# Performance work log

Hardware: AMD Instinct MI355X
Metric: run time of the kernel (lower is better)

## Reference

```python
import jax, jax.numpy as jnp
import numpy as np

B, N, HID = 1, 2048, 1024
H, WK, WV = 16, 64, 64
DH = HID // H  # 64


def setup_inputs() -> dict:
    key = jax.random.key(0)
    ks = jax.random.split(key, 10)
    s = 0.02
    return {
        "hidden_states": jax.random.normal(ks[0], (B, N, HID), jnp.float32),
        "attention_mask": jnp.ones((B, N), jnp.float32),
        "Wq": jax.random.normal(ks[1], (HID, HID), jnp.float32) * s,
        "bq": jnp.zeros((HID,), jnp.float32),
        "Wk": jax.random.normal(ks[2], (HID, HID), jnp.float32) * s,
        "bk": jnp.zeros((HID,), jnp.float32),
        "Wv": jax.random.normal(ks[3], (HID, HID), jnp.float32) * s,
        "bv": jnp.zeros((HID,), jnp.float32),
        # Conv1D(2*WK+1, DH, bias=False): weight [nx=DH, nf=2*WK+1]
        "W_rel_k": jax.random.normal(ks[4], (DH, 2 * WK + 1), jnp.float32) * s,
        # relative_pos_val: [2*WV+1, DH]
        "W_rel_v": jax.random.normal(ks[5], (2 * WV + 1, DH), jnp.float32) * s,
    }


def _attention(hidden_states, attention_mask, Wq, bq, Wk, bk, Wv, bv, W_rel_k, W_rel_v):
    b, n, _ = hidden_states.shape

    def heads(x):  # [B,N,HID] -> [B,H,N,DH]
        return x.reshape(b, n, H, DH).transpose(0, 2, 1, 3)

    q = heads(hidden_states @ Wq + bq)
    k = heads(hidden_states @ Wk + bk)
    v = heads(hidden_states @ Wv + bv)

    scores = jnp.einsum("bhid,bhjd->bhij", q, k)  # [B,H,N,N]

    # --- relative-position key bias: bias[i, j] = q_i . w_{j-i+WK} for |j-i|<=WK ---
    a_k = jnp.einsum("bhid,dw->bhiw", q, W_rel_k)  # [B,H,N,2*WK+1]
    rows = jnp.arange(n)
    slot = rows[None, :] - rows[:, None] + WK       # [N,N] relative slot j-i+WK
    valid_k = (slot >= 0) & (slot <= 2 * WK)
    bias = a_k[:, :, rows[:, None], jnp.clip(slot, 0, 2 * WK)]  # [B,H,N,N]
    scores = scores + jnp.where(valid_k, bias, 0.0)

    scores = scores / np.float32(np.sqrt(DH))  # temperature == 1.0

    # extended attention mask: (1 - mask) * dtype_min added to scores
    ext = (1.0 - attention_mask)[:, None, None, :] * jnp.finfo(scores.dtype).min
    scores = scores + ext

    probs = jax.nn.softmax(scores, axis=-1)  # [B,H,N,N]

    ctx = jnp.einsum("bhij,bhjd->bhid", probs, v)  # [B,H,N,DH]

    # --- relative-position value: band[i, r] = probs[i, i-WV+r]; ctx += band @ W_rel_v ---
    offs = jnp.arange(2 * WV + 1)
    kpos = rows[:, None] - WV + offs[None, :]       # [N, 2*WV+1] absolute key position
    valid_v = (kpos >= 0) & (kpos < n)
    band = probs[:, :, rows[:, None], jnp.clip(kpos, 0, n - 1)]  # [B,H,N,2*WV+1]
    band = jnp.where(valid_v, band, 0.0)
    ctx = ctx + jnp.einsum("bhiw,wd->bhid", band, W_rel_v)

    # merge heads -> [B,N,HID]
    return ctx.transpose(0, 2, 1, 3).reshape(b, n, HID)


def reference(hidden_states, attention_mask, Wq, bq, Wk, bk, Wv, bv, W_rel_k, W_rel_v):
    return _attention(hidden_states, attention_mask, Wq, bq, Wk, bk, Wv, bv, W_rel_k, W_rel_v)
```

## Files before the change

kernel.cpp:

```cpp
#include <hip/hip_runtime.h>
#include <hip/hip_bf16.h>

#define NSEQ 2048
#define HIDDIM 1024
#define NH 16
#define DHEAD 64
#define NW 129
#define AKS 132
#define VTS 132

typedef float          f32x4 __attribute__((ext_vector_type(4)));
typedef _Float16       f16x4 __attribute__((ext_vector_type(4)));
typedef _Float16       f16x8 __attribute__((ext_vector_type(8)));
typedef unsigned short u16x8 __attribute__((ext_vector_type(8)));
typedef unsigned short u16;

__device__ __forceinline__ float b2f(u16 u){ return __uint_as_float(((unsigned)u) << 16); }
__device__ __forceinline__ float ld_any(const void* p, long idx, int flag){
  return flag ? b2f(((const u16*)p)[idx]) : ((const float*)p)[idx];
}

static const size_t OFF_Q    = 0;
static const size_t OFF_K    = (size_t)4  << 20;
static const size_t OFF_VT   = (size_t)8  << 20;
static const size_t OFF_WT   = (size_t)12 << 20;
static const size_t OFF_AK   = (size_t)18 << 20;
static const size_t OFF_M    = OFF_AK + (size_t)NH * NSEQ * AKS * 4;
static const size_t OFF_L    = OFF_M + (size_t)2 * NH * NSEQ * 4;
static const size_t OFF_CTXP = OFF_L + (size_t)2 * NH * NSEQ * 4;
static const size_t OFF_HSF  = OFF_CTXP + (size_t)2 * NSEQ * HIDDIM * 4;
static const size_t OFF_BIAS = OFF_HSF + (size_t)NSEQ * HIDDIM * 2;
static const size_t OFF_WRK  = OFF_BIAS + 3 * 1024 * 4;
static const size_t OFF_WRV  = OFF_WRK + (size_t)DHEAD * NW * 4;
static const size_t OFF_EXT  = OFF_WRV + (size_t)NW * DHEAD * 4;

__global__ void prep_kernel(const void* __restrict__ hs,
                            const void* __restrict__ Wq, const void* __restrict__ Wk,
                            const void* __restrict__ Wv,
                            const void* __restrict__ bq, const void* __restrict__ bk,
                            const void* __restrict__ bv, const void* __restrict__ wrk,
                            const void* __restrict__ wrv, const void* __restrict__ mask,
                            _Float16* __restrict__ hsf, _Float16* __restrict__ Wt,
                            float* __restrict__ biasf, float* __restrict__ wrkf,
                            float* __restrict__ wrvf, float* __restrict__ extf){
  __shared__ __attribute__((aligned(16))) _Float16 tile[64][65];
  const int flag = (((const unsigned*)mask)[0] == 0x3F800000u) ? 0 : 1;
  const int b = blockIdx.x, t = threadIdx.x;
  if (b < 1024){
    const long base = (long)(b * 256 + t) * 8;
    f16x8 o;
    if (flag){
      const u16* src = (const u16*)hs;
#pragma unroll
      for (int e = 0; e < 8; e++) o[e] = (_Float16)b2f(src[base + e]);
    } else {
      const float* src = (const float*)hs;
#pragma unroll
      for (int e = 0; e < 8; e++) o[e] = (_Float16)src[base + e];
    }
    *(f16x8*)(hsf + base) = o;
  } else if (b < 1792){
    const int b2 = b - 1024;
    const int z = b2 >> 8, r = b2 & 255;
    const int o0 = (r & 15) * 64, k0 = (r >> 4) * 64;
    const void* src = (z == 0) ? Wq : ((z == 1) ? Wk : Wv);
    _Float16* dst = Wt + (size_t)z * 1024 * 1024;
#pragma unroll
    for (int c = 0; c < 2; c++){
      int idx = t + 256 * c;
      int rr = idx >> 3, c8 = (idx & 7) * 8;
      long off = (long)(k0 + rr) * 1024 + o0 + c8;
#pragma unroll
      for (int e = 0; e < 8; e++) tile[rr][c8 + e] = (_Float16)ld_any(src, off + e, flag);
    }
    __syncthreads();
#pragma unroll
    for (int c = 0; c < 2; c++){
      int idx = t + 256 * c;
      int orow = idx >> 3, k8 = (idx & 7) * 8;
      f16x8 v;
#pragma unroll
      for (int e = 0; e < 8; e++) v[e] = tile[k8 + e][orow];
      *(f16x8*)(dst + (size_t)(o0 + orow) * 1024 + k0 + k8) = v;
    }
  } else {
    const int idx = (b - 1792) * 256 + t;
    if (idx < 1024)            biasf[idx] = ld_any(bq, idx, flag);
    else if (idx < 2048)       biasf[idx] = ld_any(bk, idx - 1024, flag);
    else if (idx < 3072)       biasf[idx] = ld_any(bv, idx - 2048, flag);
    else if (idx < 3072 + 8256)  wrkf[idx - 3072]  = ld_any(wrk, idx - 3072, flag);
    else if (idx < 3072 + 16512) wrvf[idx - 11328] = ld_any(wrv, idx - 11328, flag);
    else if (idx < 3072 + 16512 + 2048)
      extf[idx - 19584] = (1.f - ld_any(mask, idx - 19584, flag)) * -1.0e30f;
  }
}

__launch_bounds__(256, 2)
__global__ void qkv_kernel(const _Float16* __restrict__ hsf, const _Float16* __restrict__ Wt,
                           const float* __restrict__ biasf,
                           _Float16* __restrict__ Qf, _Float16* __restrict__ Kf,
                           _Float16* __restrict__ Vtf){
  __shared__ __attribute__((aligned(16))) _Float16 As[128 * 40];
  __shared__ __attribute__((aligned(16))) _Float16 Bs[128 * 40];
  const int z = blockIdx.z;
  const _Float16* Wz = Wt + (size_t)z * 1024 * 1024;
  const int o0 = blockIdx.x * 128, m0 = blockIdx.y * 128;
  const int t = threadIdx.x, lane = t & 63, wave = t >> 6;
  const int wm = wave >> 1, wn = wave & 1;
  const int q = lane >> 4, ln = lane & 15;
  const int srow = t >> 2, scol = (t & 3) * 8;
  f32x4 acc[4][4];
#pragma unroll
  for (int a = 0; a < 4; a++)
#pragma unroll
    for (int b = 0; b < 4; b++) acc[a][b] = (f32x4){0.f, 0.f, 0.f, 0.f};

  f16x8 ar[2], br[2];
#pragma unroll
  for (int c = 0; c < 2; c++){
    ar[c] = *(const f16x8*)(hsf + (size_t)(m0 + srow + 64 * c) * 1024 + scol);
    br[c] = *(const f16x8*)(Wz + (size_t)(o0 + srow + 64 * c) * 1024 + scol);
  }
  for (int k0 = 0; k0 < 1024; k0 += 32){
#pragma unroll
    for (int c = 0; c < 2; c++){
      *(f16x8*)&As[(srow + 64 * c) * 40 + scol] = ar[c];
      *(f16x8*)&Bs[(srow + 64 * c) * 40 + scol] = br[c];
    }
    __syncthreads();
    if (k0 + 32 < 1024){
#pragma unroll
      for (int c = 0; c < 2; c++){
        ar[c] = *(const f16x8*)(hsf + (size_t)(m0 + srow + 64 * c) * 1024 + k0 + 32 + scol);
        br[c] = *(const f16x8*)(Wz + (size_t)(o0 + srow + 64 * c) * 1024 + k0 + 32 + scol);
      }
    }
    f16x8 af[4], bf[4];
#pragma unroll
    for (int mt = 0; mt < 4; mt++) af[mt] = *(const f16x8*)&As[(wm * 64 + mt * 16 + ln) * 40 + q * 8];
#pragma unroll
    for (int nt = 0; nt < 4; nt++) bf[nt] = *(const f16x8*)&Bs[(wn * 64 + nt * 16 + ln) * 40 + q * 8];
#pragma unroll
    for (int mt = 0; mt < 4; mt++)
#pragma unroll
      for (int nt = 0; nt < 4; nt++)
        acc[mt][nt] = __builtin_amdgcn_mfma_f32_16x16x32_f16(af[mt], bf[nt], acc[mt][nt], 0, 0, 0);
    __syncthreads();
  }
#pragma unroll
  for (int nt = 0; nt < 4; nt++){
    int o = o0 + wn * 64 + nt * 16 + ln;
    float bval = biasf[z * 1024 + o];
    int hh = o >> 6, dd = o & 63;
#pragma unroll
    for (int mt = 0; mt < 4; mt++){
      int nb = m0 + wm * 64 + mt * 16 + q * 4;
      if (z == 2){
        f16x4 pk;
#pragma unroll
        for (int r = 0; r < 4; r++) pk[r] = (_Float16)(acc[mt][nt][r] + bval);
        *(f16x4*)(Vtf + (size_t)(hh * 64 + dd) * 2048 + nb) = pk;
      } else {
        _Float16* dstp = (z == 0) ? Qf : Kf;
#pragma unroll
        for (int r = 0; r < 4; r++)
          dstp[(size_t)(hh * 2048 + nb + r) * 64 + dd] = (_Float16)(acc[mt][nt][r] + bval);
      }
    }
  }
}

__launch_bounds__(256, 2)
__global__ void ak_kernel(const _Float16* __restrict__ Qf, const float* __restrict__ wrkf,
                          float* __restrict__ ak){
  __shared__ __attribute__((aligned(16))) _Float16 WrkT[144 * 72];
  const int h = blockIdx.y;
  const int i0 = blockIdx.x * 128;
  const int t = threadIdx.x, lane = t & 63, wave = t >> 6;
  const int q = lane >> 4, ln = lane & 15;
  for (int c = 0; c < 36; c++){
    int idx = t + 256 * c;
    int w = idx >> 6, d = idx & 63;
    float v = (w < NW) ? wrkf[d * NW + w] : 0.f;
    WrkT[w * 72 + d] = (_Float16)v;
  }
  __syncthreads();
  f16x8 afr[2][2];
#pragma unroll
  for (int mt = 0; mt < 2; mt++){
    int row = i0 + wave * 32 + mt * 16 + ln;
#pragma unroll
    for (int ks = 0; ks < 2; ks++)
      afr[mt][ks] = *(const f16x8*)(Qf + (size_t)(h * 2048 + row) * 64 + ks * 32 + q * 8);
  }
  f32x4 acc[2][9];
#pragma unroll
  for (int a = 0; a < 2; a++)
#pragma unroll
    for (int b = 0; b < 9; b++) acc[a][b] = (f32x4){0.f, 0.f, 0.f, 0.f};
#pragma unroll
  for (int nt = 0; nt < 9; nt++){
    f16x8 bfr0 = *(const f16x8*)&WrkT[(nt * 16 + ln) * 72 + q * 8];
    f16x8 bfr1 = *(const f16x8*)&WrkT[(nt * 16 + ln) * 72 + 32 + q * 8];
#pragma unroll
    for (int mt = 0; mt < 2; mt++){
      acc[mt][nt] = __builtin_amdgcn_mfma_f32_16x16x32_f16(afr[mt][0], bfr0, acc[mt][nt], 0, 0, 0);
      acc[mt][nt] = __builtin_amdgcn_mfma_f32_16x16x32_f16(afr[mt][1], bfr1, acc[mt][nt], 0, 0, 0);
    }
  }
#pragma unroll
  for (int nt = 0; nt < 9; nt++){
    int w = nt * 16 + ln;
    if (w > 128) continue;
#pragma unroll
    for (int mt = 0; mt < 2; mt++){
      int ib = i0 + wave * 32 + mt * 16 + q * 4;
#pragma unroll
      for (int r = 0; r < 4; r++)
        ak[(size_t)(h * 2048 + ib + r) * AKS + w] = acc[mt][nt][r];
    }
  }
}

__launch_bounds__(256, 4)
__global__ void flash_kernel(const float* __restrict__ extf,
                             const _Float16* __restrict__ Qf, const _Float16* __restrict__ Kf,
                             const _Float16* __restrict__ Vtf, float* akm,
                             float* __restrict__ ctxpart, float* __restrict__ mws,
                             float* __restrict__ lws){
  __shared__ __attribute__((aligned(16))) _Float16 Ks[128 * 72];
  __shared__ __attribute__((aligned(16))) _Float16 Vts[80 * VTS];
  __shared__ __attribute__((aligned(16))) float exts[128];
  const int h = blockIdx.x, qt = blockIdx.y, jh = blockIdx.z;
  const int t = threadIdx.x, lane = t & 63, wave = t >> 6;
  const int q = lane >> 4, ln = lane & 15;
  const int ibase = qt * 64 + wave * 16;
  const int i = ibase + ln;
  f16x8 qfrag[2];
  {
    const _Float16* qrow = Qf + (size_t)(h * 2048 + i) * 64;
    qfrag[0] = *(const f16x8*)(qrow + q * 8);
    qfrag[1] = *(const f16x8*)(qrow + 32 + q * 8);
  }
  for (int k = t; k < 16 * VTS; k += 256){
    int rr = k / VTS, cc = k - rr * VTS;
    Vts[(64 + rr) * VTS + cc] = (rr == 0 && cc < 128) ? (_Float16)1.f : (_Float16)0.f;
  }
  f32x4 accc[5];
#pragma unroll
  for (int dt = 0; dt < 5; dt++) accc[dt] = (f32x4){0.f, 0.f, 0.f, 0.f};
  float m_i = -1.0e30f;
  float* akrow = akm + (size_t)(h * 2048 + i) * AKS;
  const int jbase = jh * 1024;
  const int krow = t >> 3, kcol = (t & 7) * 8;
  const int vrow = t >> 4, vcol = (t & 15) * 8;

  f16x8 kr[4], vr[4]; float er = 0.f;
#pragma unroll
  for (int c = 0; c < 4; c++){
    kr[c] = *(const f16x8*)(Kf + (size_t)(h * 2048 + jbase + krow + 32 * c) * 64 + kcol);
    vr[c] = *(const f16x8*)(Vtf + (size_t)(h * 64 + vrow + 16 * c) * 2048 + jbase + vcol);
  }
  if (t < 128) er = extf[jbase + t];

  for (int jt = 0; jt < 8; jt++){
    const int j0 = jbase + jt * 128;
#pragma unroll
    for (int c = 0; c < 4; c++){
      *(f16x8*)&Ks[(krow + 32 * c) * 72 + kcol] = kr[c];
      f16x4 lo = {vr[c][0], vr[c][1], vr[c][2], vr[c][3]};
      f16x4 hi = {vr[c][4], vr[c][5], vr[c][6], vr[c][7]};
      *(f16x4*)&Vts[(vrow + 16 * c) * VTS + vcol] = lo;
      *(f16x4*)&Vts[(vrow + 16 * c) * VTS + vcol + 4] = hi;
    }
    if (t < 128) exts[t] = er;
    __syncthreads();
    if (jt < 7){
      const int j1 = j0 + 128;
#pragma unroll
      for (int c = 0; c < 4; c++){
        kr[c] = *(const f16x8*)(Kf + (size_t)(h * 2048 + j1 + krow + 32 * c) * 64 + kcol);
        vr[c] = *(const f16x8*)(Vtf + (size_t)(h * 64 + vrow + 16 * c) * 2048 + j1 + vcol);
      }
      if (t < 128) er = extf[j1 + t];
    }
    f32x4 s[8];
#pragma unroll
    for (int mt = 0; mt < 8; mt++){
      f16x8 kf0 = *(const f16x8*)&Ks[(mt * 16 + ln) * 72 + q * 8];
      f16x8 kf1 = *(const f16x8*)&Ks[(mt * 16 + ln) * 72 + 32 + q * 8];
      f32x4 zz = (f32x4){0.f, 0.f, 0.f, 0.f};
      zz = __builtin_amdgcn_mfma_f32_16x16x32_f16(kf0, qfrag[0], zz, 0, 0, 0);
      zz = __builtin_amdgcn_mfma_f32_16x16x32_f16(kf1, qfrag[1], zz, 0, 0, 0);
      s[mt] = zz;
    }
    const bool band = (j0 <= ibase + 79) && (j0 + 127 >= ibase - 64);
#pragma unroll
    for (int mt = 0; mt < 8; mt++){
      f32x4 ev = *(const f32x4*)&exts[mt * 16 + q * 4];
#pragma unroll
      for (int r = 0; r < 4; r++){
        float x = s[mt][r];
        int w = j0 + mt * 16 + q * 4 + r - i + 64;
        if (band && (unsigned)w <= 128u){
          x = (x + akrow[w]) * 0.125f + ev[r];
          akrow[w] = x;
        } else {
          x = x * 0.125f + ev[r];
        }
        s[mt][r] = x;
      }
    }
    float tmax = -1.0e30f;
#pragma unroll
    for (int mt = 0; mt < 8; mt++)
#pragma unroll
      for (int r = 0; r < 4; r++) tmax = fmaxf(tmax, s[mt][r]);
    tmax = fmaxf(tmax, __shfl_xor(tmax, 16, 64));
    tmax = fmaxf(tmax, __shfl_xor(tmax, 32, 64));
    float mnew = fmaxf(m_i, tmax);
    float alpha = __expf(m_i - mnew);
    m_i = mnew;
#pragma unroll
    for (int dt = 0; dt < 5; dt++)
#pragma unroll
      for (int r = 0; r < 4; r++) accc[dt][r] *= alpha;
    f16x4 pf[8];
#pragma unroll
    for (int mt = 0; mt < 8; mt++)
#pragma unroll
      for (int r = 0; r < 4; r++)
        pf[mt][r] = (_Float16)__expf(s[mt][r] - mnew);
#pragma unroll
    for (int dt = 0; dt < 5; dt++){
#pragma unroll
      for (int ks = 0; ks < 8; ks++){
        f16x4 vf = *(const f16x4*)&Vts[(dt * 16 + ln) * VTS + ks * 16 + q * 4];
        accc[dt] = __builtin_amdgcn_mfma_f32_16x16x16f16(vf, pf[ks], accc[dt], 0, 0, 0);
      }
    }
    __syncthreads();
  }
  float* cdst = ctxpart + (size_t)jh * NSEQ * HIDDIM;
#pragma unroll
  for (int dt = 0; dt < 4; dt++)
    *(f32x4*)(cdst + (size_t)i * 1024 + h * 64 + dt * 16 + q * 4) = accc[dt];
  if (q == 0){
    mws[jh * NH * NSEQ + h * 2048 + i] = m_i;
    lws[jh * NH * NSEQ + h * 2048 + i] = accc[4][0];
  }
}

__launch_bounds__(256, 2)
__global__ void finish_kernel(const float* __restrict__ sband, const float* __restrict__ mws,
                              const float* __restrict__ lws, const float* __restrict__ wrvf,
                              const float* __restrict__ ctxpart, float* __restrict__ out){
  __shared__ __attribute__((aligned(16))) _Float16 WrvT[64 * 144];
  __shared__ __attribute__((aligned(16))) _Float16 pT[144 * 72];
  __shared__ __attribute__((aligned(16))) float sM[64], sIL[64], sC0[64], sC1[64];
  const int qt = blockIdx.x, h = blockIdx.y;
  const int i0 = qt * 64;
  const int t = threadIdx.x, lane = t & 63, wave = t >> 6;
  const int q = lane >> 4, ln = lane & 15;
  for (int c = 0; c < 36; c++){
    int idx = c * 256 + t;
    int w = idx >> 6, d = idx & 63;
    WrvT[d * 144 + w] = (w < NW) ? (_Float16)wrvf[w * 64 + d] : (_Float16)0.f;
  }
  if (t < 64){
    int i = i0 + t;
    float m0 = mws[h * 2048 + i],            m1 = mws[NH * NSEQ + h * 2048 + i];
    float l0 = lws[h * 2048 + i],            l1 = lws[NH * NSEQ + h * 2048 + i];
    float M = fmaxf(m0, m1);
    float a0 = __expf(m0 - M), a1 = __expf(m1 - M);
    float L = a0 * l0 + a1 * l1;
    float iL = 1.f / L;
    sM[t] = M; sIL[t] = iL; sC0[t] = a0 * iL; sC1[t] = a1 * iL;
  }
  __syncthreads();
  for (int ii = 0; ii < 16; ii++){
    int il = wave * 16 + ii;
    float Mv = sM[il], ILv = sIL[il];
    const float* srow = sband + (size_t)(h * 2048 + i0 + il) * AKS;
#pragma unroll
    for (int c = 0; c < 3; c++){
      int w = lane + 64 * c;
      if (w < 144){
        float p = (w < NW) ? __expf(srow[w] - Mv) * ILv : 0.f;
        pT[w * 72 + il] = (_Float16)p;
      }
    }
  }
  __syncthreads();
  f32x4 acc[4];
#pragma unroll
  for (int mt = 0; mt < 4; mt++) acc[mt] = (f32x4){0.f, 0.f, 0.f, 0.f};
#pragma unroll
  for (int ks = 0; ks < 9; ks++){
    f16x4 bfr;
#pragma unroll
    for (int j = 0; j < 4; j++) bfr[j] = pT[(ks * 16 + q * 4 + j) * 72 + wave * 16 + ln];
#pragma unroll
    for (int mt = 0; mt < 4; mt++){
      f16x4 afr = *(const f16x4*)&WrvT[(mt * 16 + ln) * 144 + ks * 16 + q * 4];
      acc[mt] = __builtin_amdgcn_mfma_f32_16x16x16f16(afr, bfr, acc[mt], 0, 0, 0);
    }
  }
  const int i = i0 + wave * 16 + ln;
  const float c0 = sC0[wave * 16 + ln], c1 = sC1[wave * 16 + ln];
  const float* p0 = ctxpart;
  const float* p1 = ctxpart + (size_t)NSEQ * HIDDIM;
#pragma unroll
  for (int mt = 0; mt < 4; mt++){
    size_t off = (size_t)i * 1024 + h * 64 + mt * 16 + q * 4;
    f32x4 A0 = *(const f32x4*)(p0 + off);
    f32x4 A1 = *(const f32x4*)(p1 + off);
    f32x4 o4;
#pragma unroll
    for (int r = 0; r < 4; r++) o4[r] = c0 * A0[r] + c1 * A1[r] + acc[mt][r];
    *(f32x4*)(out + off) = o4;
  }
}

extern "C" void kernel_launch(void* const* d_in, const int* in_sizes, int n_in,
                              void* d_out, int out_size, void* d_ws, size_t ws_size,
                              hipStream_t stream){
  const void* hs   = d_in[0];
  const void* mask = d_in[1];
  const void* Wq   = d_in[2];
  const void* bq   = d_in[3];
  const void* Wk   = d_in[4];
  const void* bk   = d_in[5];
  const void* Wv   = d_in[6];
  const void* bv   = d_in[7];
  const void* Wrk  = d_in[8];
  const void* Wrv  = d_in[9];
  float* out = (float*)d_out;

  char* ws = (char*)d_ws;
  _Float16* Qf    = (_Float16*)(ws + OFF_Q);
  _Float16* Kf    = (_Float16*)(ws + OFF_K);
  _Float16* Vtf   = (_Float16*)(ws + OFF_VT);
  _Float16* Wt    = (_Float16*)(ws + OFF_WT);
  float*    akp   = (float*)   (ws + OFF_AK);
  float*    mp    = (float*)   (ws + OFF_M);
  float*    lp    = (float*)   (ws + OFF_L);
  float*    ctxp  = (float*)   (ws + OFF_CTXP);
  _Float16* hsf   = (_Float16*)(ws + OFF_HSF);
  float*    biasf = (float*)   (ws + OFF_BIAS);
  float*    wrkf  = (float*)   (ws + OFF_WRK);
  float*    wrvf  = (float*)   (ws + OFF_WRV);
  float*    extf  = (float*)   (ws + OFF_EXT);

  prep_kernel  <<<dim3(1877),      256, 0, stream>>>(hs, Wq, Wk, Wv, bq, bk, bv, Wrk, Wrv, mask,
                                                     hsf, Wt, biasf, wrkf, wrvf, extf);
  qkv_kernel   <<<dim3(8, 16, 3),  256, 0, stream>>>(hsf, Wt, biasf, Qf, Kf, Vtf);
  ak_kernel    <<<dim3(16, 16),    256, 0, stream>>>(Qf, wrkf, akp);
  flash_kernel <<<dim3(16, 32, 2), 256, 0, stream>>>(extf, Qf, Kf, Vtf, akp, ctxp, mp, lp);
  finish_kernel<<<dim3(32, 16),    256, 0, stream>>>(akp, mp, lp, wrvf, ctxp, out);
}
```

Before: 211.1 us.

## Pre-swizzle K/V into MFMA fragment layout and drop LDS staging in flash

The QKV projection now writes K and V directly in a per-16-row fragment-packed layout, so the flash kernel reads MFMA operands straight from global memory and no longer stages tiles through LDS or needs block barriers. Q is pre-scaled by 1/sqrt(d)*log2e and the mask by log2e so softmax uses exp2 and the mask is folded into the MFMA accumulator init. The ones-row trick for the row sum becomes an MFMA against a constant vector, and ak_kernel reads the relative-key weights from global instead of LDS with smaller blocks. This risks more global and L2 traffic, since each wave re-reads K/V without LDS sharing.

New measurement: 226.6 us. 7.3% more time.

```diff
diff --git a/kernel.cpp b/kernel.cpp
--- a/kernel.cpp
+++ b/kernel.cpp
@@ -7,13 +7,15 @@
 #define DHEAD 64
 #define NW 129
 #define AKS 132
-#define VTS 132
+#define SCALEQ 0.18033688011112043f
+#define NLOG2E 1.442695e30f
 
 typedef float          f32x4 __attribute__((ext_vector_type(4)));
 typedef _Float16       f16x4 __attribute__((ext_vector_type(4)));
 typedef _Float16       f16x8 __attribute__((ext_vector_type(8)));
-typedef unsigned short u16x8 __attribute__((ext_vector_type(8)));
 typedef unsigned short u16;
+
+#define EXP2(x) exp2f(x)
 
 __device__ __forceinline__ float b2f(u16 u){ return __uint_as_float(((unsigned)u) << 16); }
 __device__ __forceinline__ float ld_any(const void* p, long idx, int flag){
@@ -91,15 +93,15 @@
     else if (idx < 3072 + 8256)  wrkf[idx - 3072]  = ld_any(wrk, idx - 3072, flag);
     else if (idx < 3072 + 16512) wrvf[idx - 11328] = ld_any(wrv, idx - 11328, flag);
     else if (idx < 3072 + 16512 + 2048)
-      extf[idx - 19584] = (1.f - ld_any(mask, idx - 19584, flag)) * -1.0e30f;
+      extf[idx - 19584] = (ld_any(mask, idx - 19584, flag) - 1.f) * NLOG2E;
   }
 }
 
 __launch_bounds__(256, 2)
 __global__ void qkv_kernel(const _Float16* __restrict__ hsf, const _Float16* __restrict__ Wt,
                            const float* __restrict__ biasf,
-                           _Float16* __restrict__ Qf, _Float16* __restrict__ Kf,
-                           _Float16* __restrict__ Vtf){
+                           _Float16* __restrict__ Qf, _Float16* __restrict__ Kp,
+                           _Float16* __restrict__ Vp){
   __shared__ __attribute__((aligned(16))) _Float16 As[128 * 40];
   __shared__ __attribute__((aligned(16))) _Float16 Bs[128 * 40];
   const int z = blockIdx.z;
@@ -155,82 +157,68 @@
 #pragma unroll
     for (int mt = 0; mt < 4; mt++){
       int nb = m0 + wm * 64 + mt * 16 + q * 4;
-      if (z == 2){
+      if (z == 0){
+#pragma unroll
+        for (int r = 0; r < 4; r++)
+          Qf[(size_t)(hh * 2048 + nb + r) * 64 + dd] = (_Float16)((acc[mt][nt][r] + bval) * SCALEQ);
+      } else if (z == 1){
+        size_t base = (size_t)hh * 131072 + (size_t)(nb >> 4) * 1024 + (dd >> 3) * 128 + (dd & 7);
+#pragma unroll
+        for (int r = 0; r < 4; r++)
+          Kp[base + (size_t)((q * 4 + r)) * 8] = (_Float16)(acc[mt][nt][r] + bval);
+      } else {
         f16x4 pk;
 #pragma unroll
         for (int r = 0; r < 4; r++) pk[r] = (_Float16)(acc[mt][nt][r] + bval);
-        *(f16x4*)(Vtf + (size_t)(hh * 64 + dd) * 2048 + nb) = pk;
-      } else {
-        _Float16* dstp = (z == 0) ? Qf : Kf;
-#pragma unroll
-        for (int r = 0; r < 4; r++)
-          dstp[(size_t)(hh * 2048 + nb + r) * 64 + dd] = (_Float16)(acc[mt][nt][r] + bval);
+        *(f16x4*)(Vp + (size_t)hh * 131072 + (size_t)(nb >> 4) * 1024 +
+                  (size_t)((nb >> 2) & 3) * 256 + dd * 4) = pk;
       }
     }
   }
 }
 
-__launch_bounds__(256, 2)
+__launch_bounds__(256, 4)
 __global__ void ak_kernel(const _Float16* __restrict__ Qf, const float* __restrict__ wrkf,
                           float* __restrict__ ak){
-  __shared__ __attribute__((aligned(16))) _Float16 WrkT[144 * 72];
   const int h = blockIdx.y;
-  const int i0 = blockIdx.x * 128;
   const int t = threadIdx.x, lane = t & 63, wave = t >> 6;
   const int q = lane >> 4, ln = lane & 15;
-  for (int c = 0; c < 36; c++){
-    int idx = t + 256 * c;
-    int w = idx >> 6, d = idx & 63;
-    float v = (w < NW) ? wrkf[d * NW + w] : 0.f;
-    WrkT[w * 72 + d] = (_Float16)v;
-  }
-  __syncthreads();
-  f16x8 afr[2][2];
-#pragma unroll
-  for (int mt = 0; mt < 2; mt++){
-    int row = i0 + wave * 32 + mt * 16 + ln;
-#pragma unroll
-    for (int ks = 0; ks < 2; ks++)
-      afr[mt][ks] = *(const f16x8*)(Qf + (size_t)(h * 2048 + row) * 64 + ks * 32 + q * 8);
-  }
-  f32x4 acc[2][9];
-#pragma unroll
-  for (int a = 0; a < 2; a++)
-#pragma unroll
-    for (int b = 0; b < 9; b++) acc[a][b] = (f32x4){0.f, 0.f, 0.f, 0.f};
-#pragma unroll
-  for (int nt = 0; nt < 9; nt++){
-    f16x8 bfr0 = *(const f16x8*)&WrkT[(nt * 16 + ln) * 72 + q * 8];
-    f16x8 bfr1 = *(const f16x8*)&WrkT[(nt * 16 + ln) * 72 + 32 + q * 8];
-#pragma unroll
-    for (int mt = 0; mt < 2; mt++){
-      acc[mt][nt] = __builtin_amdgcn_mfma_f32_16x16x32_f16(afr[mt][0], bfr0, acc[mt][nt], 0, 0, 0);
-      acc[mt][nt] = __builtin_amdgcn_mfma_f32_16x16x32_f16(afr[mt][1], bfr1, acc[mt][nt], 0, 0, 0);
-    }
-  }
+  const int iblk = blockIdx.x * 64 + wave * 16;
+  f16x8 afr[2];
+#pragma unroll
+  for (int ks = 0; ks < 2; ks++)
+    afr[ks] = *(const f16x8*)(Qf + (size_t)(h * 2048 + iblk + ln) * 64 + ks * 32 + q * 8);
+  f32x4 acc[9];
+#pragma unroll
+  for (int nt = 0; nt < 9; nt++) acc[nt] = (f32x4){0.f, 0.f, 0.f, 0.f};
 #pragma unroll
   for (int nt = 0; nt < 9; nt++){
     int w = nt * 16 + ln;
-    if (w > 128) continue;
-#pragma unroll
-    for (int mt = 0; mt < 2; mt++){
-      int ib = i0 + wave * 32 + mt * 16 + q * 4;
-#pragma unroll
-      for (int r = 0; r < 4; r++)
-        ak[(size_t)(h * 2048 + ib + r) * AKS + w] = acc[mt][nt][r];
-    }
+    f16x8 b0, b1;
+#pragma unroll
+    for (int e = 0; e < 8; e++){
+      b0[e] = (w < NW) ? (_Float16)wrkf[(q * 8 + e) * NW + w] : (_Float16)0.f;
+      b1[e] = (w < NW) ? (_Float16)wrkf[(32 + q * 8 + e) * NW + w] : (_Float16)0.f;
+    }
+    acc[nt] = __builtin_amdgcn_mfma_f32_16x16x32_f16(afr[0], b0, acc[nt], 0, 0, 0);
+    acc[nt] = __builtin_amdgcn_mfma_f32_16x16x32_f16(afr[1], b1, acc[nt], 0, 0, 0);
+  }
+#pragma unroll
+  for (int nt = 0; nt < 9; nt++){
+    int w = nt * 16 + ln;
+    if (w >= NW) continue;
+#pragma unroll
+    for (int r = 0; r < 4; r++)
+      ak[(size_t)(h * 2048 + iblk + q * 4 + r) * AKS + w] = acc[nt][r];
   }
 }
 
 __launch_bounds__(256, 4)
 __global__ void flash_kernel(const float* __restrict__ extf,
-                             const _Float16* __restrict__ Qf, const _Float16* __restrict__ Kf,
-                             const _Float16* __restrict__ Vtf, float* akm,
+                             const _Float16* __restrict__ Qf, const _Float16* __restrict__ Kp,
+                             const _Float16* __restrict__ Vp, float* akm,
                              float* __restrict__ ctxpart, float* __restrict__ mws,
                              float* __restrict__ lws){
-  __shared__ __attribute__((aligned(16))) _Float16 Ks[128 * 72];
-  __shared__ __attribute__((aligned(16))) _Float16 Vts[80 * VTS];
-  __shared__ __attribute__((aligned(16))) float exts[128];
   const int h = blockIdx.x, qt = blockIdx.y, jh = blockIdx.z;
   const int t = threadIdx.x, lane = t & 63, wave = t >> 6;
   const int q = lane >> 4, ln = lane & 15;
@@ -242,74 +230,40 @@
     qfrag[0] = *(const f16x8*)(qrow + q * 8);
     qfrag[1] = *(const f16x8*)(qrow + 32 + q * 8);
   }
-  for (int k = t; k < 16 * VTS; k += 256){
-    int rr = k / VTS, cc = k - rr * VTS;
-    Vts[(64 + rr) * VTS + cc] = (rr == 0 && cc < 128) ? (_Float16)1.f : (_Float16)0.f;
-  }
+  const _Float16* Kh = Kp + (size_t)h * 131072;
+  const _Float16* Vh = Vp + (size_t)h * 131072;
+  const f16x4 onesf = {(_Float16)1.f, (_Float16)1.f, (_Float16)1.f, (_Float16)1.f};
   f32x4 accc[5];
 #pragma unroll
   for (int dt = 0; dt < 5; dt++) accc[dt] = (f32x4){0.f, 0.f, 0.f, 0.f};
   float m_i = -1.0e30f;
   float* akrow = akm + (size_t)(h * 2048 + i) * AKS;
   const int jbase = jh * 1024;
-  const int krow = t >> 3, kcol = (t & 7) * 8;
-  const int vrow = t >> 4, vcol = (t & 15) * 8;
-
-  f16x8 kr[4], vr[4]; float er = 0.f;
-#pragma unroll
-  for (int c = 0; c < 4; c++){
-    kr[c] = *(const f16x8*)(Kf + (size_t)(h * 2048 + jbase + krow + 32 * c) * 64 + kcol);
-    vr[c] = *(const f16x8*)(Vtf + (size_t)(h * 64 + vrow + 16 * c) * 2048 + jbase + vcol);
-  }
-  if (t < 128) er = extf[jbase + t];
 
   for (int jt = 0; jt < 8; jt++){
     const int j0 = jbase + jt * 128;
-#pragma unroll
-    for (int c = 0; c < 4; c++){
-      *(f16x8*)&Ks[(krow + 32 * c) * 72 + kcol] = kr[c];
-      f16x4 lo = {vr[c][0], vr[c][1], vr[c][2], vr[c][3]};
-      f16x4 hi = {vr[c][4], vr[c][5], vr[c][6], vr[c][7]};
-      *(f16x4*)&Vts[(vrow + 16 * c) * VTS + vcol] = lo;
-      *(f16x4*)&Vts[(vrow + 16 * c) * VTS + vcol + 4] = hi;
-    }
-    if (t < 128) exts[t] = er;
-    __syncthreads();
-    if (jt < 7){
-      const int j1 = j0 + 128;
-#pragma unroll
-      for (int c = 0; c < 4; c++){
-        kr[c] = *(const f16x8*)(Kf + (size_t)(h * 2048 + j1 + krow + 32 * c) * 64 + kcol);
-        vr[c] = *(const f16x8*)(Vtf + (size_t)(h * 64 + vrow + 16 * c) * 2048 + j1 + vcol);
-      }
-      if (t < 128) er = extf[j1 + t];
-    }
+    const int jt16 = j0 >> 4;
     f32x4 s[8];
 #pragma unroll
     for (int mt = 0; mt < 8; mt++){
-      f16x8 kf0 = *(const f16x8*)&Ks[(mt * 16 + ln) * 72 + q * 8];
-      f16x8 kf1 = *(const f16x8*)&Ks[(mt * 16 + ln) * 72 + 32 + q * 8];
-      f32x4 zz = (f32x4){0.f, 0.f, 0.f, 0.f};
-      zz = __builtin_amdgcn_mfma_f32_16x16x32_f16(kf0, qfrag[0], zz, 0, 0, 0);
-      zz = __builtin_amdgcn_mfma_f32_16x16x32_f16(kf1, qfrag[1], zz, 0, 0, 0);
-      s[mt] = zz;
-    }
-    const bool band = (j0 <= ibase + 79) && (j0 + 127 >= ibase - 64);
-#pragma unroll
-    for (int mt = 0; mt < 8; mt++){
-      f32x4 ev = *(const f32x4*)&exts[mt * 16 + q * 4];
-#pragma unroll
-      for (int r = 0; r < 4; r++){
-        float x = s[mt][r];
-        int w = j0 + mt * 16 + q * 4 + r - i + 64;
-        if (band && (unsigned)w <= 128u){
-          x = (x + akrow[w]) * 0.125f + ev[r];
-          akrow[w] = x;
-        } else {
-          x = x * 0.125f + ev[r];
+      f32x4 ev = *(const f32x4*)(extf + j0 + mt * 16 + q * 4);
+      f16x8 kf0 = *(const f16x8*)(Kh + (size_t)(jt16 + mt) * 1024 + q * 128 + ln * 8);
+      f16x8 kf1 = *(const f16x8*)(Kh + (size_t)(jt16 + mt) * 1024 + (q + 4) * 128 + ln * 8);
+      f32x4 zz = __builtin_amdgcn_mfma_f32_16x16x32_f16(kf0, qfrag[0], ev, 0, 0, 0);
+      s[mt] = __builtin_amdgcn_mfma_f32_16x16x32_f16(kf1, qfrag[1], zz, 0, 0, 0);
+    }
+    if ((j0 <= ibase + 79) && (j0 + 127 >= ibase - 64)){
+#pragma unroll
+      for (int mt = 0; mt < 8; mt++)
+#pragma unroll
+        for (int r = 0; r < 4; r++){
+          int w = j0 + mt * 16 + q * 4 + r - i + 64;
+          if ((unsigned)w <= 128u){
+            float x = s[mt][r] + akrow[w];
+            akrow[w] = x;
+            s[mt][r] = x;
+          }
         }
-        s[mt][r] = x;
-      }
     }
     float tmax = -1.0e30f;
 #pragma unroll
@@ -319,7 +273,7 @@
     tmax = fmaxf(tmax, __shfl_xor(tmax, 16, 64));
     tmax = fmaxf(tmax, __shfl_xor(tmax, 32, 64));
     float mnew = fmaxf(m_i, tmax);
-    float alpha = __expf(m_i - mnew);
+    float alpha = EXP2(m_i - mnew);
     m_i = mnew;
 #pragma unroll
     for (int dt = 0; dt < 5; dt++)
@@ -330,16 +284,17 @@
     for (int mt = 0; mt < 8; mt++)
 #pragma unroll
       for (int r = 0; r < 4; r++)
-        pf[mt][r] = (_Float16)__expf(s[mt][r] - mnew);
-#pragma unroll
-    for (int dt = 0; dt < 5; dt++){
-#pragma unroll
-      for (int ks = 0; ks < 8; ks++){
-        f16x4 vf = *(const f16x4*)&Vts[(dt * 16 + ln) * VTS + ks * 16 + q * 4];
+        pf[mt][r] = (_Float16)EXP2(s[mt][r] - mnew);
+#pragma unroll
+    for (int ks = 0; ks < 8; ks++){
+      const _Float16* vbase = Vh + (size_t)(jt16 + ks) * 1024 + q * 256 + ln * 4;
+#pragma unroll
+      for (int dt = 0; dt < 4; dt++){
+        f16x4 vf = *(const f16x4*)(vbase + dt * 64);
         accc[dt] = __builtin_amdgcn_mfma_f32_16x16x16f16(vf, pf[ks], accc[dt], 0, 0, 0);
       }
-    }
-    __syncthreads();
+      accc[4] = __builtin_amdgcn_mfma_f32_16x16x16f16(onesf, pf[ks], accc[4], 0, 0, 0);
+    }
   }
   float* cdst = ctxpart + (size_t)jh * NSEQ * HIDDIM;
 #pragma unroll
@@ -372,7 +327,7 @@
     float m0 = mws[h * 2048 + i],            m1 = mws[NH * NSEQ + h * 2048 + i];
     float l0 = lws[h * 2048 + i],            l1 = lws[NH * NSEQ + h * 2048 + i];
     float M = fmaxf(m0, m1);
-    float a0 = __expf(m0 - M), a1 = __expf(m1 - M);
+    float a0 = EXP2(m0 - M), a1 = EXP2(m1 - M);
     float L = a0 * l0 + a1 * l1;
     float iL = 1.f / L;
     sM[t] = M; sIL[t] = iL; sC0[t] = a0 * iL; sC1[t] = a1 * iL;
@@ -380,13 +335,15 @@
   __syncthreads();
   for (int ii = 0; ii < 16; ii++){
     int il = wave * 16 + ii;
+    int i = i0 + il;
     float Mv = sM[il], ILv = sIL[il];
-    const float* srow = sband + (size_t)(h * 2048 + i0 + il) * AKS;
+    const float* srow = sband + (size_t)(h * 2048 + i) * AKS;
 #pragma unroll
     for (int c = 0; c < 3; c++){
       int w = lane + 64 * c;
       if (w < 144){
-        float p = (w < NW) ? __expf(srow[w] - Mv) * ILv : 0.f;
+        bool ok = (w < NW) && ((unsigned)(i + w - 64) < (unsigned)NSEQ);
+        float p = ok ? EXP2(srow[w] - Mv) * ILv : 0.f;
         pT[w * 72 + il] = (_Float16)p;
       }
     }
@@ -439,8 +396,8 @@
 
   char* ws = (char*)d_ws;
   _Float16* Qf    = (_Float16*)(ws + OFF_Q);
-  _Float16* Kf    = (_Float16*)(ws + OFF_K);
-  _Float16* Vtf   = (_Float16*)(ws + OFF_VT);
+  _Float16* Kp    = (_Float16*)(ws + OFF_K);
+  _Float16* Vp    = (_Float16*)(ws + OFF_VT);
   _Float16* Wt    = (_Float16*)(ws + OFF_WT);
   float*    akp   = (float*)   (ws + OFF_AK);
   float*    mp    = (float*)   (ws + OFF_M);
@@ -454,8 +411,8 @@
 
   prep_kernel  <<<dim3(1877),      256, 0, stream>>>(hs, Wq, Wk, Wv, bq, bk, bv, Wrk, Wrv, mask,
                                                      hsf, Wt, biasf, wrkf, wrvf, extf);
-  qkv_kernel   <<<dim3(8, 16, 3),  256, 0, stream>>>(hsf, Wt, biasf, Qf, Kf, Vtf);
-  ak_kernel    <<<dim3(16, 16),    256, 0, stream>>>(Qf, wrkf, akp);
-  flash_kernel <<<dim3(16, 32, 2), 256, 0, stream>>>(extf, Qf, Kf, Vtf, akp, ctxp, mp, lp);
+  qkv_kernel   <<<dim3(8, 16, 3),  256, 0, stream>>>(hsf, Wt, biasf, Qf, Kp, Vp);
+  ak_kernel    <<<dim3(32, 16),    256, 0, stream>>>(Qf, wrkf, akp);
+  flash_kernel <<<dim3(16, 32, 2), 256, 0, stream>>>(extf, Qf, Kp, Vp, akp, ctxp, mp, lp);
   finish_kernel<<<dim3(32, 16),    256, 0, stream>>>(akp, mp, lp, wrvf, ctxp, out);
 }
```
